# Kernel tuning notes

Measured on AMD Instinct MI355X. Metric: run time of the kernel, lower is better.

The kernel has to match this reference:

```python
import jax, jax.numpy as jnp
import numpy as np

B, T, F, H = 1024, 512, 40, 50


def setup_inputs() -> dict:
    key = jax.random.key(0)
    ks = jax.random.split(key, 9)
    s = 0.1
    return {
        "x": jax.random.normal(ks[0], (B, T, F), dtype=jnp.float32),
        "W_ih": jax.random.normal(ks[1], (4 * H, F), dtype=jnp.float32) * s,
        "W_hh": jax.random.normal(ks[2], (4 * H, H), dtype=jnp.float32) * s,
        "b_ih": jax.random.normal(ks[3], (4 * H,), dtype=jnp.float32) * s,
        "b_hh": jax.random.normal(ks[4], (4 * H,), dtype=jnp.float32) * s,
        "W1": jax.random.normal(ks[5], (10, H), dtype=jnp.float32) * s,
        "b1": jax.random.normal(ks[6], (10,), dtype=jnp.float32) * s,
        "W2": jax.random.normal(ks[7], (1, 10), dtype=jnp.float32) * s,
        "b2": jax.random.normal(ks[8], (1,), dtype=jnp.float32) * s,
    }


def reference(x, W_ih, W_hh, b_ih, b_hh, W1, b1, W2, b2):
    b, t, f = x.shape
    h = W_hh.shape[1]
    # Precompute input projections for all timesteps: [T, B, 4H]
    xg = jnp.einsum("btf,gf->tbg", x, W_ih) + (b_ih + b_hh)

    h0 = jnp.zeros((b, h), dtype=x.dtype)
    c0 = jnp.zeros((b, h), dtype=x.dtype).at[:, 0].set(1.0)

    def step(carry, xg_t):
        hx, cx = carry
        gates = xg_t + hx @ W_hh.T  # [B, 4H]
        i, fg, g, o = jnp.split(gates, 4, axis=-1)  # PyTorch gate order i,f,g,o
        i = jax.nn.sigmoid(i)
        fg = jax.nn.sigmoid(fg)
        g = jnp.tanh(g)
        o = jax.nn.sigmoid(o)
        cx = fg * cx + i * g
        hx = o * jnp.tanh(cx)
        return (hx, cx), None

    (hx, _), _ = jax.lax.scan(step, (h0, c0), xg)
    head = jax.nn.relu(hx @ W1.T + b1) @ W2.T + b2  # [B, 1]
    return head + x[:, -1, 0:1]
```

## Files before the change

### kernel.cpp

```cpp
#include <hip/hip_runtime.h>


constexpr int kT    = 512;
constexpr int kF    = 40;
constexpr int kH    = 50;
constexpr int kMB   = 2;
constexpr int kRowS = 104;

typedef __attribute__((ext_vector_type(8))) short bf16x8;
typedef __attribute__((ext_vector_type(4))) float f32x4;

__device__ __forceinline__ unsigned short f2bf(float f) {
    union { float f; unsigned u; } v; v.f = f;
    return (unsigned short)((v.u + 0x7FFFu + ((v.u >> 16) & 1u)) >> 16);
}
__device__ __forceinline__ float fast_sigmoid(float v) {
    return __builtin_amdgcn_rcpf(1.f + __expf(-v));
}
__device__ __forceinline__ float fast_tanh(float v) {
    return 1.f - 2.f * __builtin_amdgcn_rcpf(__expf(2.f * v) + 1.f);
}

__global__ __launch_bounds__(256, 2)
void lstm_mfma_fused(
    const float* __restrict__ x,
    const float* __restrict__ W_ih,
    const float* __restrict__ W_hh,
    const float* __restrict__ b_ih,
    const float* __restrict__ b_hh,
    const float* __restrict__ W1,
    const float* __restrict__ b1,
    const float* __restrict__ W2,
    const float* __restrict__ b2,
    float* __restrict__ out)
{
    const int tid  = threadIdx.x;
    const int lane = tid & 63;
    const int wave = tid >> 6;
    const int bb   = blockIdx.x;
    const int m16  = lane & 15;
    const int q    = lane >> 4;

    __shared__ __align__(16) short sh_comb[2][16][kRowS];
    __shared__ __align__(16) float sh_wg[4][32][4];
    __shared__ float sh_hf[kMB][kH + 2];
    __shared__ float sh_head[kMB][10];

    const int t0 = (wave == 3) ? 9 : wave * 3;
    const int NT = (wave == 3) ? 4 : 3;

    { int* z = (int*)sh_comb; for (int i = tid; i < 1664; i += 256) z[i] = 0; }

    bf16x8 wa[4][3];
    f32x4  bias4[4];
    const int uA = m16 >> 2, gA = m16 & 3;
#pragma unroll
    for (int i = 0; i < 4; ++i) {
        const int tl = t0 + i;
        const int unitA = 4 * tl + uA;
        const bool live = (i < NT) && (unitA < kH);
        const int orow = live ? (unitA + 50 * gA) : 0;
#pragma unroll
        for (int kk = 0; kk < 3; ++kk) {
            bf16x8 v;
#pragma unroll
            for (int j = 0; j < 8; ++j) {
                const int k = kk * 32 + q * 8 + j;
                float wv = 0.f;
                if (live) {
                    if (k < kF)           wv = W_ih[orow * kF + k];
                    else if (k < kF + kH) wv = W_hh[orow * kH + (k - kF)];
                }
                v[j] = (short)f2bf(wv);
            }
            wa[i][kk] = v;
        }
        const int uD = 4 * tl + q;
#pragma unroll
        for (int r = 0; r < 4; ++r)
            bias4[i][r] = (i < NT && uD < kH)
                        ? (b_ih[uD + 50 * r] + b_hh[uD + 50 * r]) : 0.f;
    }

    const int oi = lane >> 3;
    const int om = (lane >> 2) & 1;
    const int oq = lane & 3;
    const int ou = 4 * (t0 + oi) + oq;
    const bool ow = (lane < 32) && (oi < NT) && (ou < kH);
    float c    = (ow && ou == 0) ? 1.f : 0.f;
    float hreg = 0.f;

    const bool xst = (lane >= 32 && lane < 42);
    const int  fid = xst ? (wave * 10 + (lane - 32)) : 0;
    const int  xm = fid / 20, xd = fid % 20;
    const float* xrow = x + ((size_t)(bb * kMB + xm) * kT) * kF + 2 * xd;

    float2 pa = {0.f, 0.f}, pb = {0.f, 0.f};
    __syncthreads();
    if (xst) {
        float2 v0 = *(const float2*)xrow;
        unsigned pk = (unsigned)f2bf(v0.x) | ((unsigned)f2bf(v0.y) << 16);
        *(unsigned*)&sh_comb[0][xm][2 * xd] = pk;
        pa = *(const float2*)(xrow + (size_t)1 * kF);
        pb = *(const float2*)(xrow + (size_t)2 * kF);
    }
    __syncthreads();

    auto step = [&](int t, int CUR, float2& pf) {
        const short* rowp = &sh_comb[CUR][m16][0];
        bf16x8 bv0 = *(const bf16x8*)(rowp +      q * 8);
        bf16x8 bv1 = *(const bf16x8*)(rowp + 32 + q * 8);
        bf16x8 bv2 = *(const bf16x8*)(rowp + 64 + q * 8);
#pragma unroll
        for (int i = 0; i < 4; ++i) {
            if (i < NT) {
                f32x4 d = bias4[i];
                d = __builtin_amdgcn_mfma_f32_16x16x32_bf16(wa[i][0], bv0, d, 0, 0, 0);
                d = __builtin_amdgcn_mfma_f32_16x16x32_bf16(wa[i][1], bv1, d, 0, 0, 0);
                d = __builtin_amdgcn_mfma_f32_16x16x32_bf16(wa[i][2], bv2, d, 0, 0, 0);
                if (m16 < kMB)
                    *(f32x4*)&sh_wg[wave][8 * i + 4 * m16 + q][0] = d;
            }
        }
        short* nbuf = &sh_comb[CUR ^ 1][0][0];
        if (xst) {
            if (t + 1 < kT) {
                unsigned pk = (unsigned)f2bf(pf.x) | ((unsigned)f2bf(pf.y) << 16);
                *(unsigned*)&nbuf[xm * kRowS + 2 * xd] = pk;
            }
            if (t + 3 < kT)
                pf = *(const float2*)(xrow + (size_t)(t + 3) * kF);
        }
        if (ow) {
            f32x4 g = *(const f32x4*)&sh_wg[wave][lane][0];
            float i_s = fast_sigmoid(g[0]);
            float f_s = fast_sigmoid(g[1]);
            float g_t = fast_tanh   (g[2]);
            float o_s = fast_sigmoid(g[3]);
            c = fmaf(f_s, c, i_s * g_t);
            hreg = o_s * fast_tanh(c);
            if (t + 1 < kT)
                nbuf[om * kRowS + kF + ou] = (short)f2bf(hreg);
        }
        __syncthreads();
    };

    for (int t = 0; t < kT; t += 2) {
        step(t,     0, pa);
        step(t + 1, 1, pb);
    }

    if (ow) sh_hf[om][ou] = hreg;
    __syncthreads();
    if (tid < kMB * 10) {
        const int m = tid / 10, j = tid % 10;
        float acc = b1[j];
#pragma unroll
        for (int k = 0; k < kH; ++k) acc = fmaf(sh_hf[m][k], W1[j * kH + k], acc);
        sh_head[m][j] = fmaxf(acc, 0.f);
    }
    __syncthreads();
    if (tid < kMB) {
        float acc = b2[0];
#pragma unroll
        for (int j2 = 0; j2 < 10; ++j2) acc = fmaf(sh_head[tid][j2], W2[j2], acc);
        const int bidx = bb * kMB + tid;
        out[bidx] = acc + x[((size_t)bidx * kT + (kT - 1)) * kF];
    }
}

extern "C" void kernel_launch(void* const* d_in, const int* in_sizes, int n_in,
                              void* d_out, int out_size, void* d_ws, size_t ws_size,
                              hipStream_t stream) {
    const float* x    = (const float*)d_in[0];
    const float* W_ih = (const float*)d_in[1];
    const float* W_hh = (const float*)d_in[2];
    const float* b_ih = (const float*)d_in[3];
    const float* b_hh = (const float*)d_in[4];
    const float* W1   = (const float*)d_in[5];
    const float* b1   = (const float*)d_in[6];
    const float* W2   = (const float*)d_in[7];
    const float* b2   = (const float*)d_in[8];
    float* out = (float*)d_out;

    lstm_mfma_fused<<<dim3(1024 / kMB), dim3(256), 0, stream>>>(
        x, W_ih, W_hh, b_ih, b_hh, W1, b1, W2, b2, out);
}
```

Before: 370.1 us.

## Swap MFMA operand roles so gate outputs land in registers per unit

Swaps the MFMA A/B operands so the batch/timestep input becomes the A operand and the weights the B operand. Each lane then holds all four gates of one hidden unit in its accumulator registers, so the gate shuffle through shared memory and its extra read are removed. Each wave now computes all four gates for 16 units instead of a unit-interleaved gate tile. The per-step __syncthreads is replaced by an inline s_waitcnt plus s_barrier. In exchange, every wave runs 12 MFMAs per step regardless of liveness (the last wave has only 2 live units), and the activations are computed redundantly across the q lanes.

```diff
diff --git a/kernel.cpp b/kernel.cpp
--- a/kernel.cpp
+++ b/kernel.cpp
@@ -22,7 +22,7 @@
 }
 
 __global__ __launch_bounds__(256, 2)
-void lstm_mfma_fused(
+void lstm_mfma_swapped(
     const float* __restrict__ x,
     const float* __restrict__ W_ih,
     const float* __restrict__ W_hh,
@@ -41,25 +41,20 @@
     const int m16  = lane & 15;
     const int q    = lane >> 4;
 
-    __shared__ __align__(16) short sh_comb[2][16][kRowS];
-    __shared__ __align__(16) float sh_wg[4][32][4];
+    __shared__ short sh_comb[2][16][kRowS];
     __shared__ float sh_hf[kMB][kH + 2];
     __shared__ float sh_head[kMB][10];
 
-    const int t0 = (wave == 3) ? 9 : wave * 3;
-    const int NT = (wave == 3) ? 4 : 3;
+    const int u = 16 * wave + m16;
+    const bool ulive = (u < kH);
 
     { int* z = (int*)sh_comb; for (int i = tid; i < 1664; i += 256) z[i] = 0; }
 
-    bf16x8 wa[4][3];
-    f32x4  bias4[4];
-    const int uA = m16 >> 2, gA = m16 & 3;
+    bf16x8 wb[4][3];
+    float  biasv[4];
 #pragma unroll
-    for (int i = 0; i < 4; ++i) {
-        const int tl = t0 + i;
-        const int unitA = 4 * tl + uA;
-        const bool live = (i < NT) && (unitA < kH);
-        const int orow = live ? (unitA + 50 * gA) : 0;
+    for (int r = 0; r < 4; ++r) {
+        const int nrow = ulive ? (50 * r + u) : 0;
 #pragma unroll
         for (int kk = 0; kk < 3; ++kk) {
             bf16x8 v;
@@ -67,37 +62,29 @@
             for (int j = 0; j < 8; ++j) {
                 const int k = kk * 32 + q * 8 + j;
                 float wv = 0.f;
-                if (live) {
-                    if (k < kF)           wv = W_ih[orow * kF + k];
-                    else if (k < kF + kH) wv = W_hh[orow * kH + (k - kF)];
+                if (ulive) {
+                    if (k < kF)           wv = W_ih[nrow * kF + k];
+                    else if (k < kF + kH) wv = W_hh[nrow * kH + (k - kF)];
                 }
                 v[j] = (short)f2bf(wv);
             }
-            wa[i][kk] = v;
+            wb[r][kk] = v;
         }
-        const int uD = 4 * tl + q;
-#pragma unroll
-        for (int r = 0; r < 4; ++r)
-            bias4[i][r] = (i < NT && uD < kH)
-                        ? (b_ih[uD + 50 * r] + b_hh[uD + 50 * r]) : 0.f;
+        biasv[r] = ulive ? (b_ih[50 * r + u] + b_hh[50 * r + u]) : 0.f;
     }
 
-    const int oi = lane >> 3;
-    const int om = (lane >> 2) & 1;
-    const int oq = lane & 3;
-    const int ou = 4 * (t0 + oi) + oq;
-    const bool ow = (lane < 32) && (oi < NT) && (ou < kH);
-    float c    = (ow && ou == 0) ? 1.f : 0.f;
-    float hreg = 0.f;
+    float c0 = (u == 0) ? 1.f : 0.f;
+    float c1 = c0;
+    float h0 = 0.f, h1 = 0.f;
 
-    const bool xst = (lane >= 32 && lane < 42);
-    const int  fid = xst ? (wave * 10 + (lane - 32)) : 0;
+    const bool xs = (lane >= 48 && lane < 58);
+    const int  fid = xs ? (wave * 10 + (lane - 48)) : 0;
     const int  xm = fid / 20, xd = fid % 20;
     const float* xrow = x + ((size_t)(bb * kMB + xm) * kT) * kF + 2 * xd;
 
     float2 pa = {0.f, 0.f}, pb = {0.f, 0.f};
     __syncthreads();
-    if (xst) {
+    if (xs) {
         float2 v0 = *(const float2*)xrow;
         unsigned pk = (unsigned)f2bf(v0.x) | ((unsigned)f2bf(v0.y) << 16);
         *(unsigned*)&sh_comb[0][xm][2 * xd] = pk;
@@ -111,19 +98,18 @@
         bf16x8 bv0 = *(const bf16x8*)(rowp +      q * 8);
         bf16x8 bv1 = *(const bf16x8*)(rowp + 32 + q * 8);
         bf16x8 bv2 = *(const bf16x8*)(rowp + 64 + q * 8);
+        f32x4 dd[4];
 #pragma unroll
-        for (int i = 0; i < 4; ++i) {
-            if (i < NT) {
-                f32x4 d = bias4[i];
-                d = __builtin_amdgcn_mfma_f32_16x16x32_bf16(wa[i][0], bv0, d, 0, 0, 0);
-                d = __builtin_amdgcn_mfma_f32_16x16x32_bf16(wa[i][1], bv1, d, 0, 0, 0);
-                d = __builtin_amdgcn_mfma_f32_16x16x32_bf16(wa[i][2], bv2, d, 0, 0, 0);
-                if (m16 < kMB)
-                    *(f32x4*)&sh_wg[wave][8 * i + 4 * m16 + q][0] = d;
-            }
+        for (int r = 0; r < 4; ++r) {
+            f32x4 d;
+            d[0] = biasv[r]; d[1] = biasv[r]; d[2] = biasv[r]; d[3] = biasv[r];
+            d = __builtin_amdgcn_mfma_f32_16x16x32_bf16(bv0, wb[r][0], d, 0, 0, 0);
+            d = __builtin_amdgcn_mfma_f32_16x16x32_bf16(bv1, wb[r][1], d, 0, 0, 0);
+            d = __builtin_amdgcn_mfma_f32_16x16x32_bf16(bv2, wb[r][2], d, 0, 0, 0);
+            dd[r] = d;
         }
         short* nbuf = &sh_comb[CUR ^ 1][0][0];
-        if (xst) {
+        if (xs) {
             if (t + 1 < kT) {
                 unsigned pk = (unsigned)f2bf(pf.x) | ((unsigned)f2bf(pf.y) << 16);
                 *(unsigned*)&nbuf[xm * kRowS + 2 * xd] = pk;
@@ -131,18 +117,27 @@
             if (t + 3 < kT)
                 pf = *(const float2*)(xrow + (size_t)(t + 3) * kF);
         }
-        if (ow) {
-            f32x4 g = *(const f32x4*)&sh_wg[wave][lane][0];
-            float i_s = fast_sigmoid(g[0]);
-            float f_s = fast_sigmoid(g[1]);
-            float g_t = fast_tanh   (g[2]);
-            float o_s = fast_sigmoid(g[3]);
-            c = fmaf(f_s, c, i_s * g_t);
-            hreg = o_s * fast_tanh(c);
-            if (t + 1 < kT)
-                nbuf[om * kRowS + kF + ou] = (short)f2bf(hreg);
+        {
+            float i_s = fast_sigmoid(dd[0][0]);
+            float f_s = fast_sigmoid(dd[1][0]);
+            float g_t = fast_tanh   (dd[2][0]);
+            float o_s = fast_sigmoid(dd[3][0]);
+            c0 = fmaf(f_s, c0, i_s * g_t);
+            h0 = o_s * fast_tanh(c0);
         }
-        __syncthreads();
+        {
+            float i_s = fast_sigmoid(dd[0][1]);
+            float f_s = fast_sigmoid(dd[1][1]);
+            float g_t = fast_tanh   (dd[2][1]);
+            float o_s = fast_sigmoid(dd[3][1]);
+            c1 = fmaf(f_s, c1, i_s * g_t);
+            h1 = o_s * fast_tanh(c1);
+        }
+        if (q == 0 && ulive && t + 1 < kT) {
+            nbuf[0 * kRowS + kF + u] = (short)f2bf(h0);
+            nbuf[1 * kRowS + kF + u] = (short)f2bf(h1);
+        }
+        asm volatile("s_waitcnt lgkmcnt(0)\n\ts_barrier" ::: "memory");
     };
 
     for (int t = 0; t < kT; t += 2) {
@@ -150,7 +145,7 @@
         step(t + 1, 1, pb);
     }
 
-    if (ow) sh_hf[om][ou] = hreg;
+    if (q == 0 && ulive) { sh_hf[0][u] = h0; sh_hf[1][u] = h1; }
     __syncthreads();
     if (tid < kMB * 10) {
         const int m = tid / 10, j = tid % 10;
@@ -183,6 +178,6 @@
     const float* b2   = (const float*)d_in[8];
     float* out = (float*)d_out;
 
-    lstm_mfma_fused<<<dim3(1024 / kMB), dim3(256), 0, stream>>>(
+    lstm_mfma_swapped<<<dim3(1024 / kMB), dim3(256), 0, stream>>>(
         x, W_ih, W_hh, b_ih, b_hh, W1, b1, W2, b2, out);
 }
```

New measurement: 376.5 us. About the same (+1.7%).
